# Kernel optimization log

Hardware: AMD Instinct MI355X
Metric: run time of the kernel (lower is better)

The kernel has to match this reference:

```python
import jax, jax.numpy as jnp
import numpy as np

STRIDES = [8, 16, 32, 64, 128]
HW = [(100, 128), (50, 64), (25, 32), (13, 16), (7, 8)]
SCORE_THR = 0.05
IOU_THR = 0.6
MAX_DET = 1000
MAX_OUT = 100  # fixed pad size in _post_process


def _coords(h, w, stride):
    # FCOS coords_fmap2orig: center of each cell in original image coords
    sx = jnp.arange(w, dtype=jnp.float32) * stride + stride // 2
    sy = jnp.arange(h, dtype=jnp.float32) * stride + stride // 2
    yy, xx = jnp.meshgrid(sy, sx, indexing='ij')
    return jnp.stack([xx.reshape(-1), yy.reshape(-1)], axis=-1)  # [h*w, 2]


def _reshape_cat(feats):
    # list of [B,C,h,w] -> [B, sum(h*w), C]
    outs = [f.transpose(0, 2, 3, 1).reshape(f.shape[0], -1, f.shape[1]) for f in feats]
    return jnp.concatenate(outs, axis=1)


def _nms_single(scores, classes, boxes):
    # scores [N] (sorted desc), classes [N] int, boxes [N,4]; greedy DIoU-NMS
    N = scores.shape[0]
    valid = scores >= SCORE_THR
    # batched_nms: offset boxes by class so cross-class boxes never overlap
    max_coord = jnp.max(jnp.where(valid[:, None], boxes, -jnp.inf))
    offs = classes.astype(boxes.dtype) * (max_coord + 1.0)
    b = boxes + offs[:, None]
    x1, y1, x2, y2 = b[:, 0], b[:, 1], b[:, 2], b[:, 3]
    areas = (x2 - x1 + 1.0) * (y2 - y1 + 1.0)
    cx, cy = (x1 + x2) * 0.5, (y1 + y2) * 0.5
    xmin = jnp.maximum(x1[:, None], x1[None, :]); ymin = jnp.maximum(y1[:, None], y1[None, :])
    xmax = jnp.minimum(x2[:, None], x2[None, :]); ymax = jnp.minimum(y2[:, None], y2[None, :])
    inter = jnp.clip(xmax - xmin, 0) * jnp.clip(ymax - ymin, 0)
    iou = inter / (areas[:, None] + areas[None, :] - inter)
    inter_diag = (cx[:, None] - cx[None, :]) ** 2 + (cy[:, None] - cy[None, :]) ** 2
    oxmin = jnp.minimum(x1[:, None], x1[None, :]); oymin = jnp.minimum(y1[:, None], y1[None, :])
    oxmax = jnp.maximum(x2[:, None], x2[None, :]); oymax = jnp.maximum(y2[:, None], y2[None, :])
    outer_diag = (oxmax - oxmin) ** 2 + (oymax - oymin) ** 2
    diou = iou - inter_diag / jnp.maximum(outer_diag, 1e-12)
    idxs = jnp.arange(N)

    def body(i, keep):
        sup = keep[i] & (idxs > i) & (diou[i] > IOU_THR)
        return keep & (~sup)

    keep = jax.lax.fori_loop(0, N, body, valid)
    # kept boxes in descending-score order, padded with -2 to MAX_OUT
    rank = jnp.cumsum(keep) - 1
    pos = jnp.where(keep, jnp.minimum(rank, MAX_OUT), MAX_OUT)  # slot MAX_OUT is dumped
    out_s = jnp.full((MAX_OUT + 1,), -2.0, scores.dtype).at[pos].set(jnp.where(keep, scores, -2.0))[:MAX_OUT]
    out_c = jnp.full((MAX_OUT + 1,), -2, classes.dtype).at[pos].set(jnp.where(keep, classes, -2))[:MAX_OUT]
    out_b = jnp.full((MAX_OUT + 1, 4), -2.0, boxes.dtype).at[pos].set(jnp.where(keep[:, None], boxes, -2.0))[:MAX_OUT]
    return out_s, out_c, out_b


def _forward(cls_feats, reg_feats):
    cls_logits = _reshape_cat(cls_feats)          # [B, L, C]
    reg_preds = _reshape_cat(reg_feats)           # [B, L, 4]
    coords = jnp.concatenate([_coords(h, w, s) for (h, w), s in zip(HW, STRIDES)], axis=0)
    cls_preds = jax.nn.sigmoid(cls_logits)
    cls_scores = jnp.max(cls_preds, axis=-1)      # [B, L]
    cls_classes = jnp.argmax(cls_preds, axis=-1) + 1
    x1y1 = coords[None] - reg_preds[..., :2]
    x2y2 = coords[None] + reg_preds[..., 2:]
    boxes = jnp.concatenate([x1y1, x2y2], axis=-1)  # [B, L, 4]
    max_num = min(MAX_DET, cls_scores.shape[-1])
    topv, topi = jax.lax.top_k(cls_scores, max_num)  # sorted descending
    top_c = jnp.take_along_axis(cls_classes, topi, axis=1)
    top_b = jnp.take_along_axis(boxes, topi[..., None], axis=1)
    return jax.vmap(_nms_single)(topv, top_c, top_b)


def setup_inputs() -> dict:
    key = jax.random.key(0)
    ks = jax.random.split(key, 16)
    inp = {}
    C = 80
    for i, (h, w) in enumerate(HW):
        inp[f'cls{i}'] = jax.random.normal(ks[i], (16, C, h, w), dtype=jnp.float32)
        # ltrb offsets scaled so boxes are realistically sized and overlap
        inp[f'reg{i}'] = jax.random.uniform(ks[5 + i], (16, 4, h, w), dtype=jnp.float32) * 64.0
    inp['boxes_anchor'] = jax.random.normal(ks[10], (16, 100, 4), dtype=jnp.float32)
    inp['labels_anchor'] = jax.random.randint(ks[11], (16, 100), 0, 80)
    inp['score_anchor'] = jax.random.uniform(ks[12], (16, 100), dtype=jnp.float32)
    return inp


def reference(cls0, cls1, cls2, cls3, cls4, reg0, reg1, reg2, reg3, reg4,
              boxes_anchor, labels_anchor, score_anchor):
    # nms_anchor (boxes_anchor, labels_anchor, score_anchor) is consumed but
    # does not affect the output in the original forward.
    scores, classes, boxes = _forward([cls0, cls1, cls2, cls3, cls4],
                                      [reg0, reg1, reg2, reg3, reg4])
    return scores, classes, boxes
```

## Files before the change

kernel.cpp:

```cpp
#include <hip/hip_runtime.h>
#include <math.h>

typedef unsigned int u32;
typedef unsigned long long u64;

#define BB 16
#define NANCH 17064
#define NGRP 4266
#define NTOP 1000
#define NWORD 16
#define NOUT 100
#define NBIN13 8192
#define NSPLIT 17
#define CANDCAP 6144

__device__ __forceinline__ u32 fmap(float v) {
    u32 u = __float_as_uint(v);
    return (u & 0x80000000u) ? ~u : (u | 0x80000000u);
}
__device__ __forceinline__ float funmap(u32 u) {
    u32 b = (u & 0x80000000u) ? (u & 0x7FFFFFFFu) : ~u;
    return __uint_as_float(b);
}

__global__ void __launch_bounds__(256) k_anchor(
        const float* __restrict__ c0, const float* __restrict__ c1,
        const float* __restrict__ c2, const float* __restrict__ c3,
        const float* __restrict__ c4,
        const float* __restrict__ r0, const float* __restrict__ r1,
        const float* __restrict__ r2, const float* __restrict__ r3,
        const float* __restrict__ r4,
        u32* __restrict__ akey, int* __restrict__ aclass,
        float* __restrict__ abox, u32* __restrict__ ghist) {
    __shared__ u32 h1[NBIN13];
    int tid = threadIdx.x;
    int b = blockIdx.y;
    int gt = blockIdx.x * 256 + tid;
    bool valid = gt < 4 * NGRP;

    for (int i = tid; i < NBIN13; i += 256) h1[i] = 0;
    __syncthreads();

    if (valid) {
        int p = gt >> 2, cs = gt & 3;
        int a = p * 4;

        const float *cp, *rp;
        int loc, wl, h, stride, half;
        if (a < 12800)      { loc = a;         wl = 7; h = 100; stride = 8;   half = 4;  cp = c0; rp = r0; }
        else if (a < 16000) { loc = a - 12800; wl = 6; h = 50;  stride = 16;  half = 8;  cp = c1; rp = r1; }
        else if (a < 16800) { loc = a - 16000; wl = 5; h = 25;  stride = 32;  half = 16; cp = c2; rp = r2; }
        else if (a < 17008) { loc = a - 16800; wl = 4; h = 13;  stride = 64;  half = 32; cp = c3; rp = r3; }
        else                { loc = a - 17008; wl = 3; h = 7;   stride = 128; half = 64; cp = c4; rp = r4; }
        int y = loc >> wl, x = loc & ((1 << wl) - 1);
        int hw = h << wl, hwq = hw >> 2;

        const float4* cb4 = (const float4*)(cp + (size_t)b * 80 * hw +
                                            (size_t)cs * 20 * hw + loc);
        float4 buf[20];
#pragma unroll
        for (int c = 0; c < 20; ++c) buf[c] = cb4[(size_t)c * hwq];
        const float4* rb4 = (const float4*)(rp + (size_t)b * 4 * hw + loc);
        float4 gl, gt_, gr, gb;
        if (cs == 0) {
            gl = rb4[0]; gt_ = rb4[hwq]; gr = rb4[2 * hwq]; gb = rb4[3 * hwq];
        }
        __builtin_amdgcn_sched_barrier(0);

        int cbase = cs * 20;
        float m0 = buf[0].x, m1 = buf[0].y, m2 = buf[0].z, m3 = buf[0].w;
        int a0 = cbase, a1 = cbase, a2 = cbase, a3 = cbase;
#pragma unroll
        for (int c = 1; c < 20; ++c) {
            float4 u = buf[c];
            int cc = cbase + c;
            if (u.x > m0) { m0 = u.x; a0 = cc; }
            if (u.y > m1) { m1 = u.y; a1 = cc; }
            if (u.z > m2) { m2 = u.z; a2 = cc; }
            if (u.w > m3) { m3 = u.w; a3 = cc; }
        }
        {
            bool low = (cs & 1) == 0;
            float pm; int pa; bool tk;
            pm = __shfl_xor(m0, 1); pa = __shfl_xor(a0, 1);
            tk = low ? (m0 >= pm) : (m0 > pm); m0 = tk ? m0 : pm; a0 = tk ? a0 : pa;
            pm = __shfl_xor(m1, 1); pa = __shfl_xor(a1, 1);
            tk = low ? (m1 >= pm) : (m1 > pm); m1 = tk ? m1 : pm; a1 = tk ? a1 : pa;
            pm = __shfl_xor(m2, 1); pa = __shfl_xor(a2, 1);
            tk = low ? (m2 >= pm) : (m2 > pm); m2 = tk ? m2 : pm; a2 = tk ? a2 : pa;
            pm = __shfl_xor(m3, 1); pa = __shfl_xor(a3, 1);
            tk = low ? (m3 >= pm) : (m3 > pm); m3 = tk ? m3 : pm; a3 = tk ? a3 : pa;
        }
        {
            bool low = (cs & 2) == 0;
            float pm; int pa; bool tk;
            pm = __shfl_xor(m0, 2); pa = __shfl_xor(a0, 2);
            tk = low ? (m0 >= pm) : (m0 > pm); m0 = tk ? m0 : pm; a0 = tk ? a0 : pa;
            pm = __shfl_xor(m1, 2); pa = __shfl_xor(a1, 2);
            tk = low ? (m1 >= pm) : (m1 > pm); m1 = tk ? m1 : pm; a1 = tk ? a1 : pa;
            pm = __shfl_xor(m2, 2); pa = __shfl_xor(a2, 2);
            tk = low ? (m2 >= pm) : (m2 > pm); m2 = tk ? m2 : pm; a2 = tk ? a2 : pa;
            pm = __shfl_xor(m3, 2); pa = __shfl_xor(a3, 2);
            tk = low ? (m3 >= pm) : (m3 > pm); m3 = tk ? m3 : pm; a3 = tk ? a3 : pa;
        }
        if (cs == 0) {
            int idx = b * NANCH + a;
            u32 km0 = fmap(m0), km1 = fmap(m1), km2 = fmap(m2), km3 = fmap(m3);
            *(uint4*)(akey + idx) = make_uint4(km0, km1, km2, km3);
            *(int4*)(aclass + idx) = make_int4(a0 + 1, a1 + 1, a2 + 1, a3 + 1);
            atomicAdd(&h1[km0 >> 19], 1u);
            atomicAdd(&h1[km1 >> 19], 1u);
            atomicAdd(&h1[km2 >> 19], 1u);
            atomicAdd(&h1[km3 >> 19], 1u);
            float cy = (float)(y * stride + half);
            float cx0 = (float)(x * stride + half);
            float gls[4] = {gl.x, gl.y, gl.z, gl.w};
            float gts[4] = {gt_.x, gt_.y, gt_.z, gt_.w};
            float grs[4] = {gr.x, gr.y, gr.z, gr.w};
            float gbs[4] = {gb.x, gb.y, gb.z, gb.w};
#pragma unroll
            for (int k = 0; k < 4; ++k) {
                float cx = cx0 + (float)(k * stride);
                *(float4*)(abox + (size_t)(idx + k) * 4) =
                    make_float4(cx - gls[k], cy - gts[k], cx + grs[k], cy + gbs[k]);
            }
        }
    }
    __syncthreads();
    u32* gh = ghist + (size_t)b * NBIN13;
    for (int i = tid; i < NBIN13; i += 256) {
        u32 c = h1[i];
        if (c) atomicAdd(&gh[i], c);
    }
}

__global__ void __launch_bounds__(256) k_rank(
        const u32* __restrict__ akey, const u32* __restrict__ ghist,
        const int* __restrict__ aclass, const float* __restrict__ abox,
        float* __restrict__ tscore, int* __restrict__ tclass,
        float* __restrict__ tbox, u32* __restrict__ maxcU) {
    __shared__ u64 cand[CANDCAP];
    __shared__ u32 seg[256];
    __shared__ u32 binb[32];
    __shared__ int Gs;
    __shared__ u32 thrS;
    int b = blockIdx.y, s = blockIdx.x, t = threadIdx.x;
    const u32* gh = ghist + (size_t)b * NBIN13;
    const uint4* ak4 = (const uint4*)(akey + (size_t)b * NANCH);

    u32 sum = 0;
    {
        const uint4* g4 = (const uint4*)(gh + t * 32);
#pragma unroll
        for (int j = 0; j < 8; ++j) {
            uint4 q = g4[j];
            sum += q.x + q.y + q.z + q.w;
        }
    }
    seg[t] = sum;
    if (t == 0) Gs = 0;
    __syncthreads();
    for (int off = 1; off < 256; off <<= 1) {
        u32 v = seg[t];
        u32 add = (t + off < 256) ? seg[t + off] : 0u;
        __syncthreads();
        seg[t] = v + add;
        __syncthreads();
    }
    if (seg[t] >= NTOP) atomicMax(&Gs, t);
    __syncthreads();
    int G = Gs;
    u32 hi = (G < 255) ? seg[G + 1] : 0u;
    if (t < 32) binb[t] = gh[G * 32 + t];
    __syncthreads();
    if (t == 0) {
        u32 acc = hi;
        int T13 = G * 32;
        for (int i = 31; i >= 0; --i) {
            acc += binb[i];
            if (acc >= NTOP) { T13 = G * 32 + i; break; }
        }
        thrS = (u32)T13;
    }
    __syncthreads();
    u32 T = thrS;

    u32 cnt = 0;
    for (int i = t; i < NGRP; i += 256) {
        uint4 k4 = ak4[i];
        cnt += (k4.x >> 19) >= T;
        cnt += (k4.y >> 19) >= T;
        cnt += (k4.z >> 19) >= T;
        cnt += (k4.w >> 19) >= T;
    }
    __syncthreads();
    seg[t] = cnt;
    __syncthreads();
    for (int off = 1; off < 256; off <<= 1) {
        u32 v = seg[t];
        u32 add = (t >= off) ? seg[t - off] : 0u;
        __syncthreads();
        seg[t] = v + add;
        __syncthreads();
    }
    u32 pos = seg[t] - cnt;
    int C = (int)seg[255];
    if (C > CANDCAP) C = CANDCAP;
    for (int i = t; i < NGRP; i += 256) {
        uint4 k4 = ak4[i];
        u32 kk[4] = {k4.x, k4.y, k4.z, k4.w};
#pragma unroll
        for (int jj = 0; jj < 4; ++jj) {
            if ((kk[jj] >> 19) >= T) {
                if (pos < CANDCAP)
                    cand[pos] = ((u64)kk[jj] << 32) |
                                (u64)(0xFFFFFFFFu - (u32)(4 * i + jj));
                ++pos;
            }
        }
    }
    __syncthreads();

    for (int base = s * 256; base < C; base += NSPLIT * 256) {
        int i = base + t;
        bool have = i < C;
        u64 my = have ? cand[i] : 0ull;
        int q0 = 0, q1 = 0, q2 = 0, q3 = 0, q4 = 0, q5 = 0, q6 = 0, q7 = 0;
        int j = 0;
        for (; j + 8 <= C; j += 8) {
            u64 v0 = cand[j + 0], v1 = cand[j + 1];
            u64 v2 = cand[j + 2], v3 = cand[j + 3];
            u64 v4 = cand[j + 4], v5 = cand[j + 5];
            u64 v6 = cand[j + 6], v7 = cand[j + 7];
            q0 += v0 > my; q1 += v1 > my; q2 += v2 > my; q3 += v3 > my;
            q4 += v4 > my; q5 += v5 > my; q6 += v6 > my; q7 += v7 > my;
        }
        for (; j < C; ++j) q0 += cand[j] > my;
        int rank = ((q0 + q1) + (q2 + q3)) + ((q4 + q5) + (q6 + q7));
        u32 mymax = 0;
        if (have && rank < NTOP) {
            u32 a = 0xFFFFFFFFu - (u32)(my & 0xFFFFFFFFull);
            int src = b * NANCH + (int)a;
            int dst = b * NTOP + rank;
            float logit = funmap((u32)(my >> 32));
            float sc = 1.0f / (1.0f + expf(-logit));
            float b0 = abox[src * 4 + 0], b1 = abox[src * 4 + 1];
            float b2 = abox[src * 4 + 2], b3 = abox[src * 4 + 3];
            tscore[dst] = sc;
            tclass[dst] = aclass[src];
            tbox[dst * 4 + 0] = b0;
            tbox[dst * 4 + 1] = b1;
            tbox[dst * 4 + 2] = b2;
            tbox[dst * 4 + 3] = b3;
            if (sc >= 0.05f)
                mymax = fmap(fmaxf(fmaxf(b0, b1), fmaxf(b2, b3)));
        }
        for (int off = 32; off > 0; off >>= 1) {
            u32 o = (u32)__shfl_down((int)mymax, off);
            mymax = mymax > o ? mymax : o;
        }
        if ((t & 63) == 0) atomicMax(&maxcU[b], mymax);
    }
}

__global__ void k_sup(const float* __restrict__ tbox, const int* __restrict__ tclass,
                      const u32* __restrict__ maxcU, u64* __restrict__ sup) {
    int u = blockIdx.x, b = blockIdx.y;
    int ti = 0, rem = u;
    while (rem >= NWORD - ti) { rem -= NWORD - ti; ++ti; }
    int tj = ti + rem;
    int t = threadIdx.x;
    __shared__ double jx1[64], jy1[64], jx2[64], jy2[64], jcx[64], jcy[64], jar[64];
    double mc1 = (double)funmap(maxcU[b]) + 1.0;
    int j = tj * 64 + t;
    if (j < NTOP) {
        const float* bx = tbox + (size_t)(b * NTOP + j) * 4;
        double o = (double)tclass[b * NTOP + j] * mc1;
        double x1 = (double)bx[0] + o, y1 = (double)bx[1] + o;
        double x2 = (double)bx[2] + o, y2 = (double)bx[3] + o;
        jx1[t] = x1; jy1[t] = y1; jx2[t] = x2; jy2[t] = y2;
        jcx[t] = (x1 + x2) * 0.5; jcy[t] = (y1 + y2) * 0.5;
        jar[t] = (x2 - x1 + 1.0) * (y2 - y1 + 1.0);
    }
    __syncthreads();
    int i = ti * 64 + t;
    if (i >= NTOP) return;
    const float* bx = tbox + (size_t)(b * NTOP + i) * 4;
    double o = (double)tclass[b * NTOP + i] * mc1;
    double ix1 = (double)bx[0] + o, iy1 = (double)bx[1] + o;
    double ix2 = (double)bx[2] + o, iy2 = (double)bx[3] + o;
    double icx = (ix1 + ix2) * 0.5, icy = (iy1 + iy2) * 0.5;
    double iar = (ix2 - ix1 + 1.0) * (iy2 - iy1 + 1.0);
    u64 bits = 0;
    int jbase = tj * 64;
    for (int jj = 0; jj < 64; ++jj) {
        int jg = jbase + jj;
        if (jg >= NTOP) break;
        if (jg <= i) continue;
        double xm = fmax(ix1, jx1[jj]), ym = fmax(iy1, jy1[jj]);
        double xM = fmin(ix2, jx2[jj]), yM = fmin(iy2, jy2[jj]);
        double inter = fmax(xM - xm, 0.0) * fmax(yM - ym, 0.0);
        double U = iar + jar[jj] - inter;
        double dx = icx - jcx[jj], dy = icy - jcy[jj];
        double idg = dx * dx + dy * dy;
        double ox = fmax(ix2, jx2[jj]) - fmin(ix1, jx1[jj]);
        double oy = fmax(iy2, jy2[jj]) - fmin(iy1, jy1[jj]);
        double odg = fmax(ox * ox + oy * oy, 1e-12);
        if (inter * odg - idg * U > 0.6 * (U * odg)) bits |= (1ull << jj);
    }
    sup[(size_t)(b * NTOP + i) * NWORD + tj] = bits;
}

__global__ void __launch_bounds__(256) k_scan(
        const u64* __restrict__ sup, const float* __restrict__ tscore,
        const int* __restrict__ tclass, const float* __restrict__ tbox,
        float* __restrict__ out) {
    int b = blockIdx.x, tid = threadIdx.x;
    int lane = tid & 63;
    __shared__ u64 tl[2][64 * 17];
    __shared__ float sc_s[1024];
    __shared__ int kept_lds[NOUT];
    __shared__ int kept_sh;
    const u64* supb = sup + (size_t)b * NTOP * NWORD;
    for (int i = tid; i < 1024; i += 256)
        sc_s[i] = (i < NTOP) ? tscore[b * NTOP + i] : -1.0f;
    if (tid == 0) kept_sh = 0;
    for (int q = 0; q < 4; ++q) {
        int e = q * 256 + tid;
        int rr = e >> 4, w = e & 15;
        tl[0][rr * 17 + w] = (rr < NTOP) ? supb[(size_t)rr * 16 + w] : 0ull;
    }
    __syncthreads();
    u64 remw = 0;
    int kept = 0;
    for (int t = 0; t < NWORD; ++t) {
        int cur = t & 1;
        if (tid >= 64) {
            if (t + 1 < NWORD) {
                int r1 = (t + 1) * 64;
                for (int e = tid - 64; e < 1024; e += 192) {
                    int rr = r1 + (e >> 4), w = e & 15;
                    tl[cur ^ 1][(e >> 4) * 17 + w] =
                        (rr < NTOP) ? supb[(size_t)rr * 16 + w] : 0ull;
                }
            }
        } else {
            int r0 = t * 64;
            int r = r0 + lane;
            float s = sc_s[r];
            u64 vmask = __ballot(s >= 0.05f);
            u64 M = tl[cur][lane * 17 + t];
            u64 rem_t = __shfl(remw, t);
            u64 cnd = vmask & ~rem_t;
            u64 keepmask = 0;
            while (cnd) {
                int k = __ffsll(cnd) - 1;
                keepmask |= 1ull << k;
                if (lane == 0) kept_lds[kept] = r0 + k;
                ++kept;
                if (kept >= NOUT) break;
                u64 Mk = __shfl(M, k);
                cnd &= ~(Mk | (1ull << k));
            }
            if (lane < NWORD) {
                u64 km = keepmask;
                while (km) {
                    int k = __ffsll(km) - 1;
                    km &= km - 1;
                    remw |= tl[cur][k * 17 + lane];
                }
            }
            if (lane == 0) kept_sh = kept;
        }
        __syncthreads();
        if (kept_sh >= NOUT) break;
    }
    float* os = out + b * NOUT;
    float* oc = out + BB * NOUT + b * NOUT;
    float* ob = out + 2 * BB * NOUT + (size_t)b * NOUT * 4;
    for (int i = tid; i < NOUT; i += 256) { os[i] = -2.0f; oc[i] = -2.0f; }
    for (int i = tid; i < NOUT * 4; i += 256) ob[i] = -2.0f;
    __syncthreads();
    int ncopy = kept_sh < NOUT ? kept_sh : NOUT;
    for (int r = tid; r < ncopy; r += 256) {
        int i = kept_lds[r];
        os[r] = tscore[b * NTOP + i];
        oc[r] = (float)tclass[b * NTOP + i];
        ob[r * 4 + 0] = tbox[(size_t)(b * NTOP + i) * 4 + 0];
        ob[r * 4 + 1] = tbox[(size_t)(b * NTOP + i) * 4 + 1];
        ob[r * 4 + 2] = tbox[(size_t)(b * NTOP + i) * 4 + 2];
        ob[r * 4 + 3] = tbox[(size_t)(b * NTOP + i) * 4 + 3];
    }
}

extern "C" void kernel_launch(void* const* d_in, const int* in_sizes, int n_in,
                              void* d_out, int out_size, void* d_ws, size_t ws_size,
                              hipStream_t stream) {
    (void)in_sizes; (void)n_in; (void)out_size; (void)ws_size;
    const float* cls[5];
    const float* reg[5];
    for (int i = 0; i < 5; ++i) {
        cls[i] = (const float*)d_in[2 * i];
        reg[i] = (const float*)d_in[2 * i + 1];
    }
    float* out = (float*)d_out;

    char* ws = (char*)d_ws;
    u32* ghist = (u32*)ws;           ws += (size_t)BB * NBIN13 * sizeof(u32);
    u32* maxcU = (u32*)ws;           ws += 64;
    size_t zbytes = (size_t)BB * NBIN13 * sizeof(u32) + 64;
    u64* sup = (u64*)ws;             ws += (size_t)BB * NTOP * NWORD * sizeof(u64);
    u32* akey = (u32*)ws;            ws += (size_t)BB * NANCH * sizeof(u32);
    int* aclass = (int*)ws;          ws += (size_t)BB * NANCH * sizeof(int);
    float* abox = (float*)ws;        ws += (size_t)BB * NANCH * 4 * sizeof(float);
    float* tscore = (float*)ws;      ws += (size_t)BB * NTOP * sizeof(float);
    int* tclass = (int*)ws;          ws += (size_t)BB * NTOP * sizeof(int);
    float* tbox = (float*)ws;        ws += (size_t)BB * NTOP * 4 * sizeof(float);

    hipMemsetAsync(ghist, 0, zbytes, stream);

    k_anchor<<<dim3((4 * NGRP + 255) / 256, BB), 256, 0, stream>>>(
        cls[0], cls[1], cls[2], cls[3], cls[4],
        reg[0], reg[1], reg[2], reg[3], reg[4],
        akey, aclass, abox, ghist);
    k_rank<<<dim3(NSPLIT, BB), 256, 0, stream>>>(akey, ghist, aclass, abox,
                                                 tscore, tclass, tbox, maxcU);
    k_sup<<<dim3(136, BB), 64, 0, stream>>>(tbox, tclass, maxcU, sup);
    k_scan<<<BB, 256, 0, stream>>>(sup, tscore, tclass, tbox, out);
}
```

Measured before the change: 218.1 us.

## Refine top-k threshold with second-level shared histogram to shrink candidate set

Adds a second radix pass in k_rank: keys that fall in the 13-bit threshold bin are histogrammed on their next 13 bits in shared memory, which yields a 26-bit threshold much closer to the 1000th key. That shrinks the candidate list that feeds the O(C^2) rank-by-comparison loop. The candidate buffer now aliases the histogram with a smaller cap, and fewer split blocks are launched per batch. The extra histogram, scan and atomics are redundant work done in every split block, and ties at the 26-bit level could still push the candidate count near the smaller cap.

```diff
diff --git a/kernel.cpp b/kernel.cpp
--- a/kernel.cpp
+++ b/kernel.cpp
@@ -11,8 +11,8 @@
 #define NWORD 16
 #define NOUT 100
 #define NBIN13 8192
-#define NSPLIT 17
-#define CANDCAP 6144
+#define NSPLIT_R 8
+#define CANDCAP 4096
 
 __device__ __forceinline__ u32 fmap(float v) {
     u32 u = __float_as_uint(v);
@@ -139,11 +139,12 @@
         const int* __restrict__ aclass, const float* __restrict__ abox,
         float* __restrict__ tscore, int* __restrict__ tclass,
         float* __restrict__ tbox, u32* __restrict__ maxcU) {
-    __shared__ u64 cand[CANDCAP];
+    __shared__ u32 h2[NBIN13];
     __shared__ u32 seg[256];
     __shared__ u32 binb[32];
     __shared__ int Gs;
-    __shared__ u32 thrS;
+    __shared__ u32 T13s, As, thrS;
+    u64* cand = (u64*)h2;
     int b = blockIdx.y, s = blockIdx.x, t = threadIdx.x;
     const u32* gh = ghist + (size_t)b * NBIN13;
     const uint4* ak4 = (const uint4*)(akey + (size_t)b * NANCH);
@@ -174,24 +175,65 @@
     if (t < 32) binb[t] = gh[G * 32 + t];
     __syncthreads();
     if (t == 0) {
-        u32 acc = hi;
+        u32 acc = hi, A = hi;
         int T13 = G * 32;
         for (int i = 31; i >= 0; --i) {
+            A = acc;
             acc += binb[i];
             if (acc >= NTOP) { T13 = G * 32 + i; break; }
         }
-        thrS = (u32)T13;
-    }
-    __syncthreads();
-    u32 T = thrS;
+        T13s = (u32)T13; As = A;
+        Gs = 0;
+    }
+    __syncthreads();
+    u32 T13 = T13s, A = As;
+
+    for (int i = t; i < NBIN13; i += 256) h2[i] = 0;
+    __syncthreads();
+    for (int i = t; i < NGRP; i += 256) {
+        uint4 k4 = ak4[i];
+        if ((k4.x >> 19) == T13) atomicAdd(&h2[(k4.x >> 6) & (NBIN13 - 1)], 1u);
+        if ((k4.y >> 19) == T13) atomicAdd(&h2[(k4.y >> 6) & (NBIN13 - 1)], 1u);
+        if ((k4.z >> 19) == T13) atomicAdd(&h2[(k4.z >> 6) & (NBIN13 - 1)], 1u);
+        if ((k4.w >> 19) == T13) atomicAdd(&h2[(k4.w >> 6) & (NBIN13 - 1)], 1u);
+    }
+    __syncthreads();
+    u32 target = NTOP - A;
+    u32 s2 = 0;
+#pragma unroll
+    for (int j = 0; j < 32; ++j) s2 += h2[t * 32 + ((j + t) & 31)];
+    seg[t] = s2;
+    __syncthreads();
+    for (int off = 1; off < 256; off <<= 1) {
+        u32 v = seg[t];
+        u32 add = (t + off < 256) ? seg[t + off] : 0u;
+        __syncthreads();
+        seg[t] = v + add;
+        __syncthreads();
+    }
+    if (seg[t] >= target) atomicMax(&Gs, t);
+    __syncthreads();
+    int G2 = Gs;
+    u32 hi2 = (G2 < 255) ? seg[G2 + 1] : 0u;
+    if (t == 0) {
+        u32 acc = hi2;
+        int t2 = G2 * 32;
+        for (int i = 31; i >= 0; --i) {
+            acc += h2[G2 * 32 + i];
+            if (acc >= target) { t2 = G2 * 32 + i; break; }
+        }
+        thrS = (T13 << 13) | (u32)t2;
+    }
+    __syncthreads();
+    u32 thr = thrS;
 
     u32 cnt = 0;
     for (int i = t; i < NGRP; i += 256) {
         uint4 k4 = ak4[i];
-        cnt += (k4.x >> 19) >= T;
-        cnt += (k4.y >> 19) >= T;
-        cnt += (k4.z >> 19) >= T;
-        cnt += (k4.w >> 19) >= T;
+        cnt += (k4.x >> 6) >= thr;
+        cnt += (k4.y >> 6) >= thr;
+        cnt += (k4.z >> 6) >= thr;
+        cnt += (k4.w >> 6) >= thr;
     }
     __syncthreads();
     seg[t] = cnt;
@@ -211,7 +253,7 @@
         u32 kk[4] = {k4.x, k4.y, k4.z, k4.w};
 #pragma unroll
         for (int jj = 0; jj < 4; ++jj) {
-            if ((kk[jj] >> 19) >= T) {
+            if ((kk[jj] >> 6) >= thr) {
                 if (pos < CANDCAP)
                     cand[pos] = ((u64)kk[jj] << 32) |
                                 (u64)(0xFFFFFFFFu - (u32)(4 * i + jj));
@@ -221,7 +263,7 @@
     }
     __syncthreads();
 
-    for (int base = s * 256; base < C; base += NSPLIT * 256) {
+    for (int base = s * 256; base < C; base += NSPLIT_R * 256) {
         int i = base + t;
         bool have = i < C;
         u64 my = have ? cand[i] : 0ull;
@@ -423,8 +465,8 @@
         cls[0], cls[1], cls[2], cls[3], cls[4],
         reg[0], reg[1], reg[2], reg[3], reg[4],
         akey, aclass, abox, ghist);
-    k_rank<<<dim3(NSPLIT, BB), 256, 0, stream>>>(akey, ghist, aclass, abox,
-                                                 tscore, tclass, tbox, maxcU);
+    k_rank<<<dim3(NSPLIT_R, BB), 256, 0, stream>>>(akey, ghist, aclass, abox,
+                                                   tscore, tclass, tbox, maxcU);
     k_sup<<<dim3(136, BB), 64, 0, stream>>>(tbox, tclass, maxcU, sup);
     k_scan<<<BB, 256, 0, stream>>>(sup, tscore, tclass, tbox, out);
 }
```

Result: slower. 225.1 us (+3.2%).
